# Performance work log

Measured on AMD Instinct MI355X. Metric: run time of the kernel, lower is better.

Reference implementation:

```python
import jax, jax.numpy as jnp
import numpy as np

N_GENES = 20000
HIDDEN = 64
K_HOPS = 2
N_EDGES = 640000
BATCH = 32
BN_EPS = 1e-5


def setup_inputs() -> dict:
    key = jax.random.key(0)
    ks = jax.random.split(key, 8)
    B, N, d, E = BATCH, N_GENES, HIDDEN, N_EDGES
    x = jax.random.normal(ks[0], (B, N), jnp.float32)
    edge_index = jax.random.randint(ks[1], (2, E), 0, N).astype(jnp.int64)
    gene_emb = jax.random.normal(ks[2], (N, d), jnp.float32) * 0.02
    W_sg = jax.random.normal(ks[3], (d, d), jnp.float32) / np.sqrt(d).astype(np.float32)
    b_sg = jnp.zeros((d,), jnp.float32)
    W1 = jax.random.normal(ks[4], (d, 2 * d), jnp.float32) / np.sqrt(d).astype(np.float32)
    b1 = jnp.zeros((2 * d,), jnp.float32)
    gamma1 = jnp.ones((2 * d,), jnp.float32)
    beta1 = jnp.zeros((2 * d,), jnp.float32)
    W2 = jax.random.normal(ks[5], (2 * d, 1), jnp.float32) / np.sqrt(2 * d).astype(np.float32)
    b2 = jnp.zeros((1,), jnp.float32)
    return dict(x=x, edge_index=edge_index, gene_emb=gene_emb, W_sg=W_sg, b_sg=b_sg,
                W1=W1, b1=b1, gamma1=gamma1, beta1=beta1, W2=W2, b2=b2)


def _sgconv(gene_emb, src, dst, W_sg, b_sg):
    # SGConv: h = (D^{-1/2}(A+I)D^{-1/2})^K X W  on the co-expression graph
    N = gene_emb.shape[0]
    ones = jnp.ones(src.shape, gene_emb.dtype)
    deg = jax.ops.segment_sum(ones, dst, num_segments=N) + 1.0  # +1 self loop
    dinv = jax.lax.rsqrt(deg)
    ew = dinv[src] * dinv[dst]          # [E] symmetric edge norm
    self_w = (dinv * dinv)[:, None]     # [N,1] self-loop weight
    h = gene_emb
    for _ in range(K_HOPS):
        msg = h[src] * ew[:, None]      # gather + scale  [E,d]
        h = jax.ops.segment_sum(msg, dst, num_segments=N) + h * self_w
    return h @ W_sg + b_sg              # [N,d]


def reference(x, edge_index, gene_emb, W_sg, b_sg, W1, b1, gamma1, beta1, W2, b2):
    B, N = x.shape
    src, dst = edge_index[0], edge_index[1]
    h = _sgconv(gene_emb, src, dst, W_sg, b_sg)         # [N,d]
    # per-(cell, gene) state: expression scales the gene's graph embedding
    z = (x[:, :, None] * h[None, :, :]).reshape(B * N, -1)  # [B*N, d]
    # MLP block: Linear -> BatchNorm1d (train-mode batch stats) -> ReLU -> Linear
    z = z @ W1 + b1                                     # [B*N, 2d]
    mu = jnp.mean(z, axis=0)
    var = jnp.var(z, axis=0)
    z = (z - mu) * jax.lax.rsqrt(var + BN_EPS) * gamma1 + beta1
    z = jax.nn.relu(z)
    delta = (z @ W2 + b2).reshape(B, N)                 # per-gene scalar delta
    return x + delta                                    # residual post-perturbation expression
```

## Files before the change

### kernel.cpp

```cpp
#include <hip/hip_runtime.h>
#include <hip/hip_bf16.h>

#define NG 20000
#define HD 64
#define NE 640000
#define NB 32
#define D2 128
#define BN_EPS 1e-5f

__device__ __forceinline__ unsigned pack_bf16(float x, float y) {
    unsigned ux = __float_as_uint(x), uy = __float_as_uint(y);
    unsigned lo = (ux + 0x7FFFu + ((ux >> 16) & 1u)) >> 16;
    unsigned hi = (uy + 0x7FFFu + ((uy >> 16) & 1u)) >> 16;
    return (hi << 16) | lo;
}
__device__ __forceinline__ float2 unpack_bf16(unsigned g) {
    return make_float2(__uint_as_float(g << 16), __uint_as_float(g & 0xFFFF0000u));
}

__device__ __forceinline__ void acc8(uint4 v, float& a0, float& a1, float& a2, float& a3,
                                     float& a4, float& a5, float& a6, float& a7) {
    float2 t0 = unpack_bf16(v.x), t1 = unpack_bf16(v.y);
    float2 t2 = unpack_bf16(v.z), t3 = unpack_bf16(v.w);
    a0 += t0.x; a1 += t0.y; a2 += t1.x; a3 += t1.y;
    a4 += t2.x; a5 += t2.y; a6 += t3.x; a7 += t3.y;
}

#define IB_ZC 20
#define IB_S  1
#define IB_COL 79
#define IB_WC 33

__global__ __launch_bounds__(256) void k_init(const float* __restrict__ x,
                                              const float* __restrict__ W_sg,
                                              const float* __restrict__ b_sg,
                                              const float* __restrict__ W1,
                                              int* __restrict__ cnt, float* __restrict__ S,
                                              float* __restrict__ sx, float* __restrict__ sxx,
                                              float* __restrict__ Wc, float* __restrict__ bc) {
    int blk = blockIdx.x, tid = threadIdx.x;
    if (blk < IB_ZC) {
        int i = blk * 256 + tid;
        if (i < NG / 4) ((int4*)cnt)[i] = make_int4(0, 0, 0, 0);
    } else if (blk < IB_ZC + IB_S) {
        S[tid] = 0.f;
    } else if (blk < IB_ZC + IB_S + IB_COL) {
        int n = (blk - IB_ZC - IB_S) * 256 + tid;
        if (n < NG) {
            float s = 0.f, s2 = 0.f;
            #pragma unroll
            for (int b = 0; b < NB; ++b) {
                float v = x[b * NG + n];
                s += v;
                s2 = fmaf(v, v, s2);
            }
            sx[n] = s;
            sxx[n] = s2;
        }
    } else {
        int idx = (blk - IB_ZC - IB_S - IB_COL) * 256 + tid;
        if (idx < HD * D2) {
            int k = idx >> 7, c = idx & (D2 - 1);
            float acc = 0.f;
            #pragma unroll 8
            for (int j = 0; j < HD; ++j) acc += W_sg[k * HD + j] * W1[j * D2 + c];
            Wc[idx] = acc;
        } else if (idx < HD * D2 + D2) {
            int c = idx - HD * D2;
            float acc = 0.f;
            #pragma unroll 8
            for (int j = 0; j < HD; ++j) acc += b_sg[j] * W1[j * D2 + c];
            bc[c] = acc;
        }
    }
}


__global__ void k_scatter(const int* __restrict__ src, const int* __restrict__ dst,
                          int* __restrict__ cnt, unsigned short* __restrict__ srcs) {
    int e4 = blockIdx.x * blockDim.x + threadIdx.x;
    int4 s = ((const int4*)src)[e4];
    int4 d = ((const int4*)dst)[e4];
    srcs[(d.x << 7) + atomicAdd(&cnt[d.x], 1)] = (unsigned short)s.x;
    srcs[(d.y << 7) + atomicAdd(&cnt[d.y], 1)] = (unsigned short)s.y;
    srcs[(d.z << 7) + atomicAdd(&cnt[d.z], 1)] = (unsigned short)s.z;
    srcs[(d.w << 7) + atomicAdd(&cnt[d.w], 1)] = (unsigned short)s.w;
}


__global__ __launch_bounds__(256) void k_pre(const float* __restrict__ emb,
                                             const int* __restrict__ cnt,
                                             unsigned* __restrict__ g0) {
    int i = blockIdx.x * blockDim.x + threadIdx.x;
    float dv = rsqrtf((float)cnt[i >> 3] + 1.0f);
    float4 a = ((const float4*)emb)[i * 2];
    float4 b = ((const float4*)emb)[i * 2 + 1];
    uint4 o;
    o.x = pack_bf16(a.x * dv, a.y * dv);
    o.y = pack_bf16(a.z * dv, a.w * dv);
    o.z = pack_bf16(b.x * dv, b.y * dv);
    o.w = pack_bf16(b.z * dv, b.w * dv);
    ((uint4*)g0)[i] = o;
}


__global__ __launch_bounds__(256) void k_gather1(const unsigned short* __restrict__ srcs,
                                                 const int* __restrict__ cnt,
                                                 const unsigned* __restrict__ g,
                                                 unsigned* __restrict__ outb) {
    int n = blockIdx.x * 32 + (threadIdx.x >> 3);
    int l = threadIdx.x & 7;
    const uint4* gp = (const uint4*)g + l;
    int len = cnt[n];
    const unsigned short* row = srcs + ((size_t)n << 7);
    uint4 sv = gp[(size_t)n * 8];
    float a0, a1, a2, a3, a4, a5, a6, a7;
    {
        float2 t0 = unpack_bf16(sv.x), t1 = unpack_bf16(sv.y);
        float2 t2 = unpack_bf16(sv.z), t3 = unpack_bf16(sv.w);
        a0 = t0.x; a1 = t0.y; a2 = t1.x; a3 = t1.y;
        a4 = t2.x; a5 = t2.y; a6 = t3.x; a7 = t3.y;
    }
    int j = 0;
    for (; j + 8 <= len; j += 8) {
        uint4 iw = *(const uint4*)(row + j);
        int i0 = iw.x & 0xFFFF, i1 = iw.x >> 16, i2 = iw.y & 0xFFFF, i3 = iw.y >> 16;
        int i4 = iw.z & 0xFFFF, i5 = iw.z >> 16, i6 = iw.w & 0xFFFF, i7 = iw.w >> 16;
        uint4 v0 = gp[(size_t)i0 * 8], v1 = gp[(size_t)i1 * 8];
        uint4 v2 = gp[(size_t)i2 * 8], v3 = gp[(size_t)i3 * 8];
        uint4 v4 = gp[(size_t)i4 * 8], v5 = gp[(size_t)i5 * 8];
        uint4 v6 = gp[(size_t)i6 * 8], v7 = gp[(size_t)i7 * 8];
        acc8(v0, a0, a1, a2, a3, a4, a5, a6, a7);
        acc8(v1, a0, a1, a2, a3, a4, a5, a6, a7);
        acc8(v2, a0, a1, a2, a3, a4, a5, a6, a7);
        acc8(v3, a0, a1, a2, a3, a4, a5, a6, a7);
        acc8(v4, a0, a1, a2, a3, a4, a5, a6, a7);
        acc8(v5, a0, a1, a2, a3, a4, a5, a6, a7);
        acc8(v6, a0, a1, a2, a3, a4, a5, a6, a7);
        acc8(v7, a0, a1, a2, a3, a4, a5, a6, a7);
    }
    for (; j < len; ++j) {
        uint4 v = gp[(size_t)row[j] * 8];
        acc8(v, a0, a1, a2, a3, a4, a5, a6, a7);
    }
    float dv = rsqrtf((float)len + 1.0f);
    float sc = dv * dv;
    uint4 o;
    o.x = pack_bf16(a0 * sc, a1 * sc);
    o.y = pack_bf16(a2 * sc, a3 * sc);
    o.z = pack_bf16(a4 * sc, a5 * sc);
    o.w = pack_bf16(a6 * sc, a7 * sc);
    ((uint4*)outb)[(size_t)n * 8 + l] = o;
}


__global__ __launch_bounds__(256) void k_hop2ps(const unsigned short* __restrict__ srcs,
                                                const int* __restrict__ cnt,
                                                const unsigned* __restrict__ g,
                                                const float* __restrict__ Wc,
                                                const float* __restrict__ bc,
                                                const float* __restrict__ sx,
                                                const float* __restrict__ sxx,
                                                float* __restrict__ p,
                                                float* __restrict__ S) {
    __shared__ float lWc[HD * D2];
    __shared__ float lt[HD * 32];
    int tid = threadIdx.x;
    int n0 = blockIdx.x * 32;

    for (int i = tid; i < HD * D2 / 4; i += 256)
        ((float4*)lWc)[i] = ((const float4*)Wc)[i];

    {
        int r = tid >> 3, l = tid & 7;
        int n = n0 + r;
        const uint4* gp = (const uint4*)g + l;
        int len = cnt[n];
        const unsigned short* row = srcs + ((size_t)n << 7);
        uint4 sv = gp[(size_t)n * 8];
        float a0, a1, a2, a3, a4, a5, a6, a7;
        {
            float2 t0 = unpack_bf16(sv.x), t1 = unpack_bf16(sv.y);
            float2 t2 = unpack_bf16(sv.z), t3 = unpack_bf16(sv.w);
            a0 = t0.x; a1 = t0.y; a2 = t1.x; a3 = t1.y;
            a4 = t2.x; a5 = t2.y; a6 = t3.x; a7 = t3.y;
        }
        int j = 0;
        for (; j + 8 <= len; j += 8) {
            uint4 iw = *(const uint4*)(row + j);
            int i0 = iw.x & 0xFFFF, i1 = iw.x >> 16, i2 = iw.y & 0xFFFF, i3 = iw.y >> 16;
            int i4 = iw.z & 0xFFFF, i5 = iw.z >> 16, i6 = iw.w & 0xFFFF, i7 = iw.w >> 16;
            uint4 v0 = gp[(size_t)i0 * 8], v1 = gp[(size_t)i1 * 8];
            uint4 v2 = gp[(size_t)i2 * 8], v3 = gp[(size_t)i3 * 8];
            uint4 v4 = gp[(size_t)i4 * 8], v5 = gp[(size_t)i5 * 8];
            uint4 v6 = gp[(size_t)i6 * 8], v7 = gp[(size_t)i7 * 8];
            acc8(v0, a0, a1, a2, a3, a4, a5, a6, a7);
            acc8(v1, a0, a1, a2, a3, a4, a5, a6, a7);
            acc8(v2, a0, a1, a2, a3, a4, a5, a6, a7);
            acc8(v3, a0, a1, a2, a3, a4, a5, a6, a7);
            acc8(v4, a0, a1, a2, a3, a4, a5, a6, a7);
            acc8(v5, a0, a1, a2, a3, a4, a5, a6, a7);
            acc8(v6, a0, a1, a2, a3, a4, a5, a6, a7);
            acc8(v7, a0, a1, a2, a3, a4, a5, a6, a7);
        }
        for (; j < len; ++j) {
            uint4 v = gp[(size_t)row[j] * 8];
            acc8(v, a0, a1, a2, a3, a4, a5, a6, a7);
        }
        float dv = rsqrtf((float)len + 1.0f);
        int kb = l * 8;
        lt[(kb + 0) * 32 + r] = a0 * dv;
        lt[(kb + 1) * 32 + r] = a1 * dv;
        lt[(kb + 2) * 32 + r] = a2 * dv;
        lt[(kb + 3) * 32 + r] = a3 * dv;
        lt[(kb + 4) * 32 + r] = a4 * dv;
        lt[(kb + 5) * 32 + r] = a5 * dv;
        lt[(kb + 6) * 32 + r] = a6 * dv;
        lt[(kb + 7) * 32 + r] = a7 * dv;
    }
    __syncthreads();

    int cg = tid & 31;
    int rg = tid >> 5;
    float acc[4][4];
    #pragma unroll
    for (int i = 0; i < 4; ++i)
        #pragma unroll
        for (int j = 0; j < 4; ++j) acc[i][j] = 0.f;

    #pragma unroll 4
    for (int k = 0; k < HD; ++k) {
        float4 wv = *(const float4*)&lWc[k * D2 + cg * 4];
        float4 hv = *(const float4*)&lt[k * 32 + rg * 4];
        acc[0][0] = fmaf(hv.x, wv.x, acc[0][0]);
        acc[0][1] = fmaf(hv.x, wv.y, acc[0][1]);
        acc[0][2] = fmaf(hv.x, wv.z, acc[0][2]);
        acc[0][3] = fmaf(hv.x, wv.w, acc[0][3]);
        acc[1][0] = fmaf(hv.y, wv.x, acc[1][0]);
        acc[1][1] = fmaf(hv.y, wv.y, acc[1][1]);
        acc[1][2] = fmaf(hv.y, wv.z, acc[1][2]);
        acc[1][3] = fmaf(hv.y, wv.w, acc[1][3]);
        acc[2][0] = fmaf(hv.z, wv.x, acc[2][0]);
        acc[2][1] = fmaf(hv.z, wv.y, acc[2][1]);
        acc[2][2] = fmaf(hv.z, wv.z, acc[2][2]);
        acc[2][3] = fmaf(hv.z, wv.w, acc[2][3]);
        acc[3][0] = fmaf(hv.w, wv.x, acc[3][0]);
        acc[3][1] = fmaf(hv.w, wv.y, acc[3][1]);
        acc[3][2] = fmaf(hv.w, wv.z, acc[3][2]);
        acc[3][3] = fmaf(hv.w, wv.w, acc[3][3]);
    }

    float4 bcv = ((const float4*)bc)[cg];
    float s1[4] = {0.f, 0.f, 0.f, 0.f};
    float s2[4] = {0.f, 0.f, 0.f, 0.f};
    #pragma unroll
    for (int i = 0; i < 4; ++i) {
        int rr = rg * 4 + i;
        float xs = sx[n0 + rr], xss = sxx[n0 + rr];
        float4 o;
        o.x = acc[i][0] + bcv.x;
        o.y = acc[i][1] + bcv.y;
        o.z = acc[i][2] + bcv.z;
        o.w = acc[i][3] + bcv.w;
        s1[0] = fmaf(o.x, xs, s1[0]);  s2[0] = fmaf(o.x * o.x, xss, s2[0]);
        s1[1] = fmaf(o.y, xs, s1[1]);  s2[1] = fmaf(o.y * o.y, xss, s2[1]);
        s1[2] = fmaf(o.z, xs, s1[2]);  s2[2] = fmaf(o.z * o.z, xss, s2[2]);
        s1[3] = fmaf(o.w, xs, s1[3]);  s2[3] = fmaf(o.w * o.w, xss, s2[3]);
        ((float4*)(p + (size_t)(n0 + rr) * D2))[cg] = o;
    }

    __syncthreads();
    *(float4*)&lt[rg * D2 + cg * 4]        = make_float4(s1[0], s1[1], s1[2], s1[3]);
    *(float4*)&lt[1024 + rg * D2 + cg * 4] = make_float4(s2[0], s2[1], s2[2], s2[3]);
    __syncthreads();
    if (tid < D2) {
        float a = 0.f, b = 0.f;
        #pragma unroll
        for (int g2 = 0; g2 < 8; ++g2) {
            a += lt[g2 * D2 + tid];
            b += lt[1024 + g2 * D2 + tid];
        }
        atomicAdd(&S[tid], a);
        atomicAdd(&S[D2 + tid], b);
    }
}

#define FN 64

__global__ __launch_bounds__(256) void k_final(const float* __restrict__ x,
                                               const float* __restrict__ p,
                                               const float* __restrict__ S,
                                               const float* __restrict__ gamma1,
                                               const float* __restrict__ beta1,
                                               const float* __restrict__ W2,
                                               const float* __restrict__ b2,
                                               float* __restrict__ out) {
    __shared__ float lp[FN * 129];
    __shared__ float ls[D2], lo[D2], lw[D2];
    int tid = threadIdx.x;
    int n0 = blockIdx.x * FN;
    if (tid < D2) {
        const float inv = 1.0f / (float)(NB * NG);
        float m1 = S[tid] * inv;
        float m2 = S[D2 + tid] * inv;
        float a = gamma1[tid] * rsqrtf(m2 - m1 * m1 + BN_EPS);
        ls[tid] = a;
        lo[tid] = beta1[tid] - m1 * a;
        lw[tid] = W2[tid];
    }
    for (int i = tid; i < FN * D2 / 4; i += 256) {
        int row = i >> 5, c4 = i & 31;
        int n = n0 + row;
        float4 v = (n < NG) ? ((const float4*)(p + (size_t)n * D2))[c4]
                            : make_float4(0.f, 0.f, 0.f, 0.f);
        float* dp = lp + row * 129 + c4 * 4;
        dp[0] = v.x; dp[1] = v.y; dp[2] = v.z; dp[3] = v.w;
    }
    __syncthreads();
    int nl = tid & 63;
    int n = n0 + nl;
    if (n >= NG) return;
    int bbase = (tid >> 6) * 8;
    const float* prow = lp + nl * 129;
    float b2v = b2[0];
    float xv[8], acc[8];
    #pragma unroll
    for (int bi = 0; bi < 8; ++bi) {
        xv[bi] = x[(bbase + bi) * NG + n];
        acc[bi] = 0.f;
    }
    #pragma unroll 8
    for (int c = 0; c < D2; ++c) {
        float ps = prow[c] * ls[c];
        float ocv = lo[c];
        float wv = lw[c];
        #pragma unroll
        for (int bi = 0; bi < 8; ++bi) {
            float v = fmaxf(fmaf(xv[bi], ps, ocv), 0.f);
            acc[bi] = fmaf(v, wv, acc[bi]);
        }
    }
    #pragma unroll
    for (int bi = 0; bi < 8; ++bi)
        out[(bbase + bi) * NG + n] = xv[bi] + acc[bi] + b2v;
}

extern "C" void kernel_launch(void* const* d_in, const int* in_sizes, int n_in,
                              void* d_out, int out_size, void* d_ws, size_t ws_size,
                              hipStream_t stream) {
    const float* x        = (const float*)d_in[0];
    const int*   ei       = (const int*)d_in[1];
    const float* gene_emb = (const float*)d_in[2];
    const float* W_sg     = (const float*)d_in[3];
    const float* b_sg     = (const float*)d_in[4];
    const float* W1       = (const float*)d_in[5];
    const float* gamma1   = (const float*)d_in[7];
    const float* beta1    = (const float*)d_in[8];
    const float* W2       = (const float*)d_in[9];
    const float* b2       = (const float*)d_in[10];
    float* out = (float*)d_out;

    const int* src = ei;
    const int* dst = ei + NE;

    char* base = (char*)d_ws;
    unsigned short* srcs = (unsigned short*)base;
    int*      cnt      = (int*)(base + (size_t)NG * 128 * 2);
    unsigned* g0       = (unsigned*)(cnt + NG);
    unsigned* g1       = g0 + NG * 32;
    float*    Wc       = (float*)(g1 + NG * 32);
    float*    bc       = Wc + HD * D2;
    float*    p        = bc + D2;
    float*    sx       = p + (size_t)NG * D2;
    float*    sxx      = sx + NG;
    float*    S        = sxx + NG;

    k_init<<<IB_ZC + IB_S + IB_COL + IB_WC, 256, 0, stream>>>(x, W_sg, b_sg, W1,
                                                              cnt, S, sx, sxx, Wc, bc);
    k_scatter<<<NE / 4 / 256, 256, 0, stream>>>(src, dst, cnt, srcs);
    k_pre<<<NG * HD / 8 / 256, 256, 0, stream>>>(gene_emb, cnt, g0);

    k_gather1<<<NG / 32, 256, 0, stream>>>(srcs, cnt, g0, g1);
    k_hop2ps<<<NG / 32, 256, 0, stream>>>(srcs, cnt, g1, Wc, bc, sx, sxx, p, S);

    k_final<<<(NG + FN - 1) / FN, 256, 0, stream>>>(x, p, S, gamma1, beta1, W2, b2, out);
}
```

Baseline: 174.0 us.

## Fuse all pipeline stages into one cooperative persistent kernel with grid syncs

Replaces six separate kernel launches (init, scatter, degree-normalize, hop-1 gather, hop-2 gather plus projection and statistics, final MLP) with one persistent cooperative kernel. Stages are separated by grid-wide syncs and each stage uses grid-stride loops over its work. The aim is to remove launch gaps and inter-kernel drain and fill time. In exchange, grid.sync has its own cost and occupancy is capped by the 40KB shared buffer and the launch bounds. Grid size is derived from occupancy assuming 256 CUs.

```diff
diff --git a/kernel.cpp b/kernel.cpp
--- a/kernel.cpp
+++ b/kernel.cpp
@@ -1,5 +1,8 @@
 #include <hip/hip_runtime.h>
+#include <hip/hip_cooperative_groups.h>
 #include <hip/hip_bf16.h>
+
+namespace cg = cooperative_groups;
 
 #define NG 20000
 #define HD 64
@@ -7,6 +10,9 @@
 #define NB 32
 #define D2 128
 #define BN_EPS 1e-5f
+#define FN 64
+#define NT32 625
+#define NFT 313
 
 __device__ __forceinline__ unsigned pack_bf16(float x, float y) {
     unsigned ux = __float_as_uint(x), uy = __float_as_uint(y);
@@ -17,7 +23,6 @@
 __device__ __forceinline__ float2 unpack_bf16(unsigned g) {
     return make_float2(__uint_as_float(g << 16), __uint_as_float(g & 0xFFFF0000u));
 }
-
 __device__ __forceinline__ void acc8(uint4 v, float& a0, float& a1, float& a2, float& a3,
                                      float& a4, float& a5, float& a6, float& a7) {
     float2 t0 = unpack_bf16(v.x), t1 = unpack_bf16(v.y);
@@ -26,101 +31,15 @@
     a4 += t2.x; a5 += t2.y; a6 += t3.x; a7 += t3.y;
 }
 
-#define IB_ZC 20
-#define IB_S  1
-#define IB_COL 79
-#define IB_WC 33
-
-__global__ __launch_bounds__(256) void k_init(const float* __restrict__ x,
-                                              const float* __restrict__ W_sg,
-                                              const float* __restrict__ b_sg,
-                                              const float* __restrict__ W1,
-                                              int* __restrict__ cnt, float* __restrict__ S,
-                                              float* __restrict__ sx, float* __restrict__ sxx,
-                                              float* __restrict__ Wc, float* __restrict__ bc) {
-    int blk = blockIdx.x, tid = threadIdx.x;
-    if (blk < IB_ZC) {
-        int i = blk * 256 + tid;
-        if (i < NG / 4) ((int4*)cnt)[i] = make_int4(0, 0, 0, 0);
-    } else if (blk < IB_ZC + IB_S) {
-        S[tid] = 0.f;
-    } else if (blk < IB_ZC + IB_S + IB_COL) {
-        int n = (blk - IB_ZC - IB_S) * 256 + tid;
-        if (n < NG) {
-            float s = 0.f, s2 = 0.f;
-            #pragma unroll
-            for (int b = 0; b < NB; ++b) {
-                float v = x[b * NG + n];
-                s += v;
-                s2 = fmaf(v, v, s2);
-            }
-            sx[n] = s;
-            sxx[n] = s2;
-        }
-    } else {
-        int idx = (blk - IB_ZC - IB_S - IB_COL) * 256 + tid;
-        if (idx < HD * D2) {
-            int k = idx >> 7, c = idx & (D2 - 1);
-            float acc = 0.f;
-            #pragma unroll 8
-            for (int j = 0; j < HD; ++j) acc += W_sg[k * HD + j] * W1[j * D2 + c];
-            Wc[idx] = acc;
-        } else if (idx < HD * D2 + D2) {
-            int c = idx - HD * D2;
-            float acc = 0.f;
-            #pragma unroll 8
-            for (int j = 0; j < HD; ++j) acc += b_sg[j] * W1[j * D2 + c];
-            bc[c] = acc;
-        }
-    }
-}
-
-
-__global__ void k_scatter(const int* __restrict__ src, const int* __restrict__ dst,
-                          int* __restrict__ cnt, unsigned short* __restrict__ srcs) {
-    int e4 = blockIdx.x * blockDim.x + threadIdx.x;
-    int4 s = ((const int4*)src)[e4];
-    int4 d = ((const int4*)dst)[e4];
-    srcs[(d.x << 7) + atomicAdd(&cnt[d.x], 1)] = (unsigned short)s.x;
-    srcs[(d.y << 7) + atomicAdd(&cnt[d.y], 1)] = (unsigned short)s.y;
-    srcs[(d.z << 7) + atomicAdd(&cnt[d.z], 1)] = (unsigned short)s.z;
-    srcs[(d.w << 7) + atomicAdd(&cnt[d.w], 1)] = (unsigned short)s.w;
-}
-
-
-__global__ __launch_bounds__(256) void k_pre(const float* __restrict__ emb,
-                                             const int* __restrict__ cnt,
-                                             unsigned* __restrict__ g0) {
-    int i = blockIdx.x * blockDim.x + threadIdx.x;
-    float dv = rsqrtf((float)cnt[i >> 3] + 1.0f);
-    float4 a = ((const float4*)emb)[i * 2];
-    float4 b = ((const float4*)emb)[i * 2 + 1];
-    uint4 o;
-    o.x = pack_bf16(a.x * dv, a.y * dv);
-    o.y = pack_bf16(a.z * dv, a.w * dv);
-    o.z = pack_bf16(b.x * dv, b.y * dv);
-    o.w = pack_bf16(b.z * dv, b.w * dv);
-    ((uint4*)g0)[i] = o;
-}
-
-
-__global__ __launch_bounds__(256) void k_gather1(const unsigned short* __restrict__ srcs,
-                                                 const int* __restrict__ cnt,
-                                                 const unsigned* __restrict__ g,
-                                                 unsigned* __restrict__ outb) {
-    int n = blockIdx.x * 32 + (threadIdx.x >> 3);
-    int l = threadIdx.x & 7;
-    const uint4* gp = (const uint4*)g + l;
-    int len = cnt[n];
-    const unsigned short* row = srcs + ((size_t)n << 7);
+__device__ __forceinline__ void gather_node(const unsigned short* __restrict__ row, int len,
+                                            const uint4* __restrict__ gp, int n,
+                                            float& a0, float& a1, float& a2, float& a3,
+                                            float& a4, float& a5, float& a6, float& a7) {
     uint4 sv = gp[(size_t)n * 8];
-    float a0, a1, a2, a3, a4, a5, a6, a7;
-    {
-        float2 t0 = unpack_bf16(sv.x), t1 = unpack_bf16(sv.y);
-        float2 t2 = unpack_bf16(sv.z), t3 = unpack_bf16(sv.w);
-        a0 = t0.x; a1 = t0.y; a2 = t1.x; a3 = t1.y;
-        a4 = t2.x; a5 = t2.y; a6 = t3.x; a7 = t3.y;
-    }
+    float2 t0 = unpack_bf16(sv.x), t1 = unpack_bf16(sv.y);
+    float2 t2 = unpack_bf16(sv.z), t3 = unpack_bf16(sv.w);
+    a0 = t0.x; a1 = t0.y; a2 = t1.x; a3 = t1.y;
+    a4 = t2.x; a5 = t2.y; a6 = t3.x; a7 = t3.y;
     int j = 0;
     for (; j + 8 <= len; j += 8) {
         uint4 iw = *(const uint4*)(row + j);
@@ -143,206 +62,243 @@
         uint4 v = gp[(size_t)row[j] * 8];
         acc8(v, a0, a1, a2, a3, a4, a5, a6, a7);
     }
-    float dv = rsqrtf((float)len + 1.0f);
-    float sc = dv * dv;
-    uint4 o;
-    o.x = pack_bf16(a0 * sc, a1 * sc);
-    o.y = pack_bf16(a2 * sc, a3 * sc);
-    o.z = pack_bf16(a4 * sc, a5 * sc);
-    o.w = pack_bf16(a6 * sc, a7 * sc);
-    ((uint4*)outb)[(size_t)n * 8 + l] = o;
-}
-
-
-__global__ __launch_bounds__(256) void k_hop2ps(const unsigned short* __restrict__ srcs,
-                                                const int* __restrict__ cnt,
-                                                const unsigned* __restrict__ g,
-                                                const float* __restrict__ Wc,
-                                                const float* __restrict__ bc,
-                                                const float* __restrict__ sx,
-                                                const float* __restrict__ sxx,
-                                                float* __restrict__ p,
-                                                float* __restrict__ S) {
-    __shared__ float lWc[HD * D2];
-    __shared__ float lt[HD * 32];
-    int tid = threadIdx.x;
-    int n0 = blockIdx.x * 32;
+}
+
+__global__ __launch_bounds__(256, 4) void k_all(
+        const float* __restrict__ x, const int* __restrict__ src, const int* __restrict__ dst,
+        const float* __restrict__ emb, const float* __restrict__ W_sg,
+        const float* __restrict__ b_sg, const float* __restrict__ W1,
+        const float* __restrict__ gamma1, const float* __restrict__ beta1,
+        const float* __restrict__ W2, const float* __restrict__ b2,
+        unsigned short* __restrict__ srcs, int* __restrict__ cnt,
+        unsigned* __restrict__ g0, unsigned* __restrict__ g1,
+        float* __restrict__ Wc, float* __restrict__ bc, float* __restrict__ p,
+        float* __restrict__ sx, float* __restrict__ sxx, float* __restrict__ S,
+        float* __restrict__ out) {
+    cg::grid_group grid = cg::this_grid();
+    int tid = threadIdx.x, bid = blockIdx.x, G = gridDim.x;
+    int gt = bid * 256 + tid, GT = G * 256;
+
+    __shared__ __align__(16) char smem[40960];
+    float* lWc = (float*)smem;
+    float* lt  = (float*)(smem + 32768);
+    float* lp  = (float*)smem;
+    float* ls_ = (float*)(smem + 33024);
+    float* lo_ = ls_ + D2;
+    float* lw_ = lo_ + D2;
+
+    for (int i = gt; i < NG / 4; i += GT) ((int4*)cnt)[i] = make_int4(0, 0, 0, 0);
+    for (int i = gt; i < 2 * D2; i += GT) S[i] = 0.f;
+    for (int n = gt; n < NG; n += GT) {
+        float s = 0.f, s2 = 0.f;
+        #pragma unroll
+        for (int b = 0; b < NB; ++b) {
+            float v = x[b * NG + n];
+            s += v;
+            s2 = fmaf(v, v, s2);
+        }
+        sx[n] = s;
+        sxx[n] = s2;
+    }
+    for (int idx = gt; idx < HD * D2 + D2; idx += GT) {
+        if (idx < HD * D2) {
+            int k = idx >> 7, c = idx & (D2 - 1);
+            float acc = 0.f;
+            #pragma unroll 8
+            for (int j = 0; j < HD; ++j) acc += W_sg[k * HD + j] * W1[j * D2 + c];
+            Wc[idx] = acc;
+        } else {
+            int c = idx - HD * D2;
+            float acc = 0.f;
+            #pragma unroll 8
+            for (int j = 0; j < HD; ++j) acc += b_sg[j] * W1[j * D2 + c];
+            bc[c] = acc;
+        }
+    }
+    grid.sync();
+
+    for (int e4 = gt; e4 < NE / 4; e4 += GT) {
+        int4 s = ((const int4*)src)[e4];
+        int4 d = ((const int4*)dst)[e4];
+        srcs[(d.x << 7) + atomicAdd(&cnt[d.x], 1)] = (unsigned short)s.x;
+        srcs[(d.y << 7) + atomicAdd(&cnt[d.y], 1)] = (unsigned short)s.y;
+        srcs[(d.z << 7) + atomicAdd(&cnt[d.z], 1)] = (unsigned short)s.z;
+        srcs[(d.w << 7) + atomicAdd(&cnt[d.w], 1)] = (unsigned short)s.w;
+    }
+    grid.sync();
+
+    for (int i = gt; i < NG * HD / 8; i += GT) {
+        float dv = rsqrtf((float)cnt[i >> 3] + 1.0f);
+        float4 a = ((const float4*)emb)[i * 2];
+        float4 b = ((const float4*)emb)[i * 2 + 1];
+        uint4 o;
+        o.x = pack_bf16(a.x * dv, a.y * dv);
+        o.y = pack_bf16(a.z * dv, a.w * dv);
+        o.z = pack_bf16(b.x * dv, b.y * dv);
+        o.w = pack_bf16(b.z * dv, b.w * dv);
+        ((uint4*)g0)[i] = o;
+    }
+    grid.sync();
+
+    {
+        int r = tid >> 3, l = tid & 7;
+        const uint4* gp = (const uint4*)g0 + l;
+        for (int t = bid; t < NT32; t += G) {
+            int n = t * 32 + r;
+            int len = cnt[n];
+            float a0, a1, a2, a3, a4, a5, a6, a7;
+            gather_node(srcs + ((size_t)n << 7), len, gp, n, a0, a1, a2, a3, a4, a5, a6, a7);
+            float dv = rsqrtf((float)len + 1.0f);
+            float sc = dv * dv;
+            uint4 o;
+            o.x = pack_bf16(a0 * sc, a1 * sc);
+            o.y = pack_bf16(a2 * sc, a3 * sc);
+            o.z = pack_bf16(a4 * sc, a5 * sc);
+            o.w = pack_bf16(a6 * sc, a7 * sc);
+            ((uint4*)g1)[(size_t)n * 8 + l] = o;
+        }
+    }
+    grid.sync();
 
     for (int i = tid; i < HD * D2 / 4; i += 256)
         ((float4*)lWc)[i] = ((const float4*)Wc)[i];
-
     {
         int r = tid >> 3, l = tid & 7;
-        int n = n0 + r;
-        const uint4* gp = (const uint4*)g + l;
-        int len = cnt[n];
-        const unsigned short* row = srcs + ((size_t)n << 7);
-        uint4 sv = gp[(size_t)n * 8];
-        float a0, a1, a2, a3, a4, a5, a6, a7;
-        {
-            float2 t0 = unpack_bf16(sv.x), t1 = unpack_bf16(sv.y);
-            float2 t2 = unpack_bf16(sv.z), t3 = unpack_bf16(sv.w);
-            a0 = t0.x; a1 = t0.y; a2 = t1.x; a3 = t1.y;
-            a4 = t2.x; a5 = t2.y; a6 = t3.x; a7 = t3.y;
-        }
-        int j = 0;
-        for (; j + 8 <= len; j += 8) {
-            uint4 iw = *(const uint4*)(row + j);
-            int i0 = iw.x & 0xFFFF, i1 = iw.x >> 16, i2 = iw.y & 0xFFFF, i3 = iw.y >> 16;
-            int i4 = iw.z & 0xFFFF, i5 = iw.z >> 16, i6 = iw.w & 0xFFFF, i7 = iw.w >> 16;
-            uint4 v0 = gp[(size_t)i0 * 8], v1 = gp[(size_t)i1 * 8];
-            uint4 v2 = gp[(size_t)i2 * 8], v3 = gp[(size_t)i3 * 8];
-            uint4 v4 = gp[(size_t)i4 * 8], v5 = gp[(size_t)i5 * 8];
-            uint4 v6 = gp[(size_t)i6 * 8], v7 = gp[(size_t)i7 * 8];
-            acc8(v0, a0, a1, a2, a3, a4, a5, a6, a7);
-            acc8(v1, a0, a1, a2, a3, a4, a5, a6, a7);
-            acc8(v2, a0, a1, a2, a3, a4, a5, a6, a7);
-            acc8(v3, a0, a1, a2, a3, a4, a5, a6, a7);
-            acc8(v4, a0, a1, a2, a3, a4, a5, a6, a7);
-            acc8(v5, a0, a1, a2, a3, a4, a5, a6, a7);
-            acc8(v6, a0, a1, a2, a3, a4, a5, a6, a7);
-            acc8(v7, a0, a1, a2, a3, a4, a5, a6, a7);
-        }
-        for (; j < len; ++j) {
-            uint4 v = gp[(size_t)row[j] * 8];
-            acc8(v, a0, a1, a2, a3, a4, a5, a6, a7);
-        }
-        float dv = rsqrtf((float)len + 1.0f);
-        int kb = l * 8;
-        lt[(kb + 0) * 32 + r] = a0 * dv;
-        lt[(kb + 1) * 32 + r] = a1 * dv;
-        lt[(kb + 2) * 32 + r] = a2 * dv;
-        lt[(kb + 3) * 32 + r] = a3 * dv;
-        lt[(kb + 4) * 32 + r] = a4 * dv;
-        lt[(kb + 5) * 32 + r] = a5 * dv;
-        lt[(kb + 6) * 32 + r] = a6 * dv;
-        lt[(kb + 7) * 32 + r] = a7 * dv;
-    }
-    __syncthreads();
-
-    int cg = tid & 31;
-    int rg = tid >> 5;
-    float acc[4][4];
-    #pragma unroll
-    for (int i = 0; i < 4; ++i)
-        #pragma unroll
-        for (int j = 0; j < 4; ++j) acc[i][j] = 0.f;
-
-    #pragma unroll 4
-    for (int k = 0; k < HD; ++k) {
-        float4 wv = *(const float4*)&lWc[k * D2 + cg * 4];
-        float4 hv = *(const float4*)&lt[k * 32 + rg * 4];
-        acc[0][0] = fmaf(hv.x, wv.x, acc[0][0]);
-        acc[0][1] = fmaf(hv.x, wv.y, acc[0][1]);
-        acc[0][2] = fmaf(hv.x, wv.z, acc[0][2]);
-        acc[0][3] = fmaf(hv.x, wv.w, acc[0][3]);
-        acc[1][0] = fmaf(hv.y, wv.x, acc[1][0]);
-        acc[1][1] = fmaf(hv.y, wv.y, acc[1][1]);
-        acc[1][2] = fmaf(hv.y, wv.z, acc[1][2]);
-        acc[1][3] = fmaf(hv.y, wv.w, acc[1][3]);
-        acc[2][0] = fmaf(hv.z, wv.x, acc[2][0]);
-        acc[2][1] = fmaf(hv.z, wv.y, acc[2][1]);
-        acc[2][2] = fmaf(hv.z, wv.z, acc[2][2]);
-        acc[2][3] = fmaf(hv.z, wv.w, acc[2][3]);
-        acc[3][0] = fmaf(hv.w, wv.x, acc[3][0]);
-        acc[3][1] = fmaf(hv.w, wv.y, acc[3][1]);
-        acc[3][2] = fmaf(hv.w, wv.z, acc[3][2]);
-        acc[3][3] = fmaf(hv.w, wv.w, acc[3][3]);
-    }
-
-    float4 bcv = ((const float4*)bc)[cg];
-    float s1[4] = {0.f, 0.f, 0.f, 0.f};
-    float s2[4] = {0.f, 0.f, 0.f, 0.f};
-    #pragma unroll
-    for (int i = 0; i < 4; ++i) {
-        int rr = rg * 4 + i;
-        float xs = sx[n0 + rr], xss = sxx[n0 + rr];
-        float4 o;
-        o.x = acc[i][0] + bcv.x;
-        o.y = acc[i][1] + bcv.y;
-        o.z = acc[i][2] + bcv.z;
-        o.w = acc[i][3] + bcv.w;
-        s1[0] = fmaf(o.x, xs, s1[0]);  s2[0] = fmaf(o.x * o.x, xss, s2[0]);
-        s1[1] = fmaf(o.y, xs, s1[1]);  s2[1] = fmaf(o.y * o.y, xss, s2[1]);
-        s1[2] = fmaf(o.z, xs, s1[2]);  s2[2] = fmaf(o.z * o.z, xss, s2[2]);
-        s1[3] = fmaf(o.w, xs, s1[3]);  s2[3] = fmaf(o.w * o.w, xss, s2[3]);
-        ((float4*)(p + (size_t)(n0 + rr) * D2))[cg] = o;
-    }
-
-    __syncthreads();
-    *(float4*)&lt[rg * D2 + cg * 4]        = make_float4(s1[0], s1[1], s1[2], s1[3]);
-    *(float4*)&lt[1024 + rg * D2 + cg * 4] = make_float4(s2[0], s2[1], s2[2], s2[3]);
-    __syncthreads();
-    if (tid < D2) {
-        float a = 0.f, b = 0.f;
-        #pragma unroll
-        for (int g2 = 0; g2 < 8; ++g2) {
-            a += lt[g2 * D2 + tid];
-            b += lt[1024 + g2 * D2 + tid];
-        }
-        atomicAdd(&S[tid], a);
-        atomicAdd(&S[D2 + tid], b);
-    }
-}
-
-#define FN 64
-
-__global__ __launch_bounds__(256) void k_final(const float* __restrict__ x,
-                                               const float* __restrict__ p,
-                                               const float* __restrict__ S,
-                                               const float* __restrict__ gamma1,
-                                               const float* __restrict__ beta1,
-                                               const float* __restrict__ W2,
-                                               const float* __restrict__ b2,
-                                               float* __restrict__ out) {
-    __shared__ float lp[FN * 129];
-    __shared__ float ls[D2], lo[D2], lw[D2];
-    int tid = threadIdx.x;
-    int n0 = blockIdx.x * FN;
+        int cgc = tid & 31, rg = tid >> 5;
+        const uint4* gp = (const uint4*)g1 + l;
+        float s1[4] = {0.f, 0.f, 0.f, 0.f};
+        float s2[4] = {0.f, 0.f, 0.f, 0.f};
+        for (int t = bid; t < NT32; t += G) {
+            int n0 = t * 32;
+            __syncthreads();
+            {
+                int n = n0 + r;
+                int len = cnt[n];
+                float a0, a1, a2, a3, a4, a5, a6, a7;
+                gather_node(srcs + ((size_t)n << 7), len, gp, n, a0, a1, a2, a3, a4, a5, a6, a7);
+                float dv = rsqrtf((float)len + 1.0f);
+                int kb = l * 8;
+                lt[(kb + 0) * 32 + r] = a0 * dv;
+                lt[(kb + 1) * 32 + r] = a1 * dv;
+                lt[(kb + 2) * 32 + r] = a2 * dv;
+                lt[(kb + 3) * 32 + r] = a3 * dv;
+                lt[(kb + 4) * 32 + r] = a4 * dv;
+                lt[(kb + 5) * 32 + r] = a5 * dv;
+                lt[(kb + 6) * 32 + r] = a6 * dv;
+                lt[(kb + 7) * 32 + r] = a7 * dv;
+            }
+            __syncthreads();
+            float acc[4][4];
+            #pragma unroll
+            for (int i = 0; i < 4; ++i)
+                #pragma unroll
+                for (int j = 0; j < 4; ++j) acc[i][j] = 0.f;
+            #pragma unroll 4
+            for (int k = 0; k < HD; ++k) {
+                float4 wv = *(const float4*)&lWc[k * D2 + cgc * 4];
+                float4 hv = *(const float4*)&lt[k * 32 + rg * 4];
+                acc[0][0] = fmaf(hv.x, wv.x, acc[0][0]);
+                acc[0][1] = fmaf(hv.x, wv.y, acc[0][1]);
+                acc[0][2] = fmaf(hv.x, wv.z, acc[0][2]);
+                acc[0][3] = fmaf(hv.x, wv.w, acc[0][3]);
+                acc[1][0] = fmaf(hv.y, wv.x, acc[1][0]);
+                acc[1][1] = fmaf(hv.y, wv.y, acc[1][1]);
+                acc[1][2] = fmaf(hv.y, wv.z, acc[1][2]);
+                acc[1][3] = fmaf(hv.y, wv.w, acc[1][3]);
+                acc[2][0] = fmaf(hv.z, wv.x, acc[2][0]);
+                acc[2][1] = fmaf(hv.z, wv.y, acc[2][1]);
+                acc[2][2] = fmaf(hv.z, wv.z, acc[2][2]);
+                acc[2][3] = fmaf(hv.z, wv.w, acc[2][3]);
+                acc[3][0] = fmaf(hv.w, wv.x, acc[3][0]);
+                acc[3][1] = fmaf(hv.w, wv.y, acc[3][1]);
+                acc[3][2] = fmaf(hv.w, wv.z, acc[3][2]);
+                acc[3][3] = fmaf(hv.w, wv.w, acc[3][3]);
+            }
+            float4 bcv = ((const float4*)bc)[cgc];
+            #pragma unroll
+            for (int i = 0; i < 4; ++i) {
+                int rr = rg * 4 + i;
+                float xs = sx[n0 + rr], xss = sxx[n0 + rr];
+                float4 o;
+                o.x = acc[i][0] + bcv.x;
+                o.y = acc[i][1] + bcv.y;
+                o.z = acc[i][2] + bcv.z;
+                o.w = acc[i][3] + bcv.w;
+                s1[0] = fmaf(o.x, xs, s1[0]);  s2[0] = fmaf(o.x * o.x, xss, s2[0]);
+                s1[1] = fmaf(o.y, xs, s1[1]);  s2[1] = fmaf(o.y * o.y, xss, s2[1]);
+                s1[2] = fmaf(o.z, xs, s1[2]);  s2[2] = fmaf(o.z * o.z, xss, s2[2]);
+                s1[3] = fmaf(o.w, xs, s1[3]);  s2[3] = fmaf(o.w * o.w, xss, s2[3]);
+                ((float4*)(p + (size_t)(n0 + rr) * D2))[cgc] = o;
+            }
+        }
+        __syncthreads();
+        *(float4*)&lt[rg * D2 + cgc * 4]        = make_float4(s1[0], s1[1], s1[2], s1[3]);
+        *(float4*)&lt[1024 + rg * D2 + cgc * 4] = make_float4(s2[0], s2[1], s2[2], s2[3]);
+        __syncthreads();
+        if (tid < D2) {
+            float a = 0.f, b = 0.f;
+            #pragma unroll
+            for (int g2 = 0; g2 < 8; ++g2) {
+                a += lt[g2 * D2 + tid];
+                b += lt[1024 + g2 * D2 + tid];
+            }
+            atomicAdd(&S[tid], a);
+            atomicAdd(&S[D2 + tid], b);
+        }
+    }
+    grid.sync();
+
     if (tid < D2) {
         const float inv = 1.0f / (float)(NB * NG);
         float m1 = S[tid] * inv;
         float m2 = S[D2 + tid] * inv;
         float a = gamma1[tid] * rsqrtf(m2 - m1 * m1 + BN_EPS);
-        ls[tid] = a;
-        lo[tid] = beta1[tid] - m1 * a;
-        lw[tid] = W2[tid];
-    }
-    for (int i = tid; i < FN * D2 / 4; i += 256) {
-        int row = i >> 5, c4 = i & 31;
-        int n = n0 + row;
-        float4 v = (n < NG) ? ((const float4*)(p + (size_t)n * D2))[c4]
-                            : make_float4(0.f, 0.f, 0.f, 0.f);
-        float* dp = lp + row * 129 + c4 * 4;
-        dp[0] = v.x; dp[1] = v.y; dp[2] = v.z; dp[3] = v.w;
-    }
-    __syncthreads();
-    int nl = tid & 63;
-    int n = n0 + nl;
-    if (n >= NG) return;
-    int bbase = (tid >> 6) * 8;
-    const float* prow = lp + nl * 129;
-    float b2v = b2[0];
-    float xv[8], acc[8];
-    #pragma unroll
-    for (int bi = 0; bi < 8; ++bi) {
-        xv[bi] = x[(bbase + bi) * NG + n];
-        acc[bi] = 0.f;
-    }
-    #pragma unroll 8
-    for (int c = 0; c < D2; ++c) {
-        float ps = prow[c] * ls[c];
-        float ocv = lo[c];
-        float wv = lw[c];
-        #pragma unroll
-        for (int bi = 0; bi < 8; ++bi) {
-            float v = fmaxf(fmaf(xv[bi], ps, ocv), 0.f);
-            acc[bi] = fmaf(v, wv, acc[bi]);
-        }
-    }
-    #pragma unroll
-    for (int bi = 0; bi < 8; ++bi)
-        out[(bbase + bi) * NG + n] = xv[bi] + acc[bi] + b2v;
+        ls_[tid] = a;
+        lo_[tid] = beta1[tid] - m1 * a;
+        lw_[tid] = W2[tid];
+    }
+    {
+        int nl = tid & 63;
+        int bbase = (tid >> 6) * 8;
+        float b2v = b2[0];
+        for (int t = bid; t < NFT; t += G) {
+            int n0 = t * FN;
+            __syncthreads();
+            for (int i = tid; i < FN * D2 / 4; i += 256) {
+                int row = i >> 5, c4 = i & 31;
+                int n = n0 + row;
+                float4 v = (n < NG) ? ((const float4*)(p + (size_t)n * D2))[c4]
+                                    : make_float4(0.f, 0.f, 0.f, 0.f);
+                float* dp = lp + row * 129 + c4 * 4;
+                dp[0] = v.x; dp[1] = v.y; dp[2] = v.z; dp[3] = v.w;
+            }
+            __syncthreads();
+            int n = n0 + nl;
+            if (n < NG) {
+                const float* prow = lp + nl * 129;
+                float xv[8], acc[8];
+                #pragma unroll
+                for (int bi = 0; bi < 8; ++bi) {
+                    xv[bi] = x[(bbase + bi) * NG + n];
+                    acc[bi] = 0.f;
+                }
+                #pragma unroll 8
+                for (int c = 0; c < D2; ++c) {
+                    float ps = prow[c] * ls_[c];
+                    float ocv = lo_[c];
+                    float wv = lw_[c];
+                    #pragma unroll
+                    for (int bi = 0; bi < 8; ++bi) {
+                        float v = fmaxf(fmaf(xv[bi], ps, ocv), 0.f);
+                        acc[bi] = fmaf(v, wv, acc[bi]);
+                    }
+                }
+                #pragma unroll
+                for (int bi = 0; bi < 8; ++bi)
+                    out[(bbase + bi) * NG + n] = xv[bi] + acc[bi] + b2v;
+            }
+        }
+    }
 }
 
 extern "C" void kernel_launch(void* const* d_in, const int* in_sizes, int n_in,
@@ -375,13 +331,18 @@
     float*    sxx      = sx + NG;
     float*    S        = sxx + NG;
 
-    k_init<<<IB_ZC + IB_S + IB_COL + IB_WC, 256, 0, stream>>>(x, W_sg, b_sg, W1,
-                                                              cnt, S, sx, sxx, Wc, bc);
-    k_scatter<<<NE / 4 / 256, 256, 0, stream>>>(src, dst, cnt, srcs);
-    k_pre<<<NG * HD / 8 / 256, 256, 0, stream>>>(gene_emb, cnt, g0);
-
-    k_gather1<<<NG / 32, 256, 0, stream>>>(srcs, cnt, g0, g1);
-    k_hop2ps<<<NG / 32, 256, 0, stream>>>(srcs, cnt, g1, Wc, bc, sx, sxx, p, S);
-
-    k_final<<<(NG + FN - 1) / FN, 256, 0, stream>>>(x, p, S, gamma1, beta1, W2, b2, out);
-}
+    int bpc = 0;
+    hipOccupancyMaxActiveBlocksPerMultiprocessor(&bpc, k_all, 256, 0);
+    if (bpc < 1) bpc = 1;
+    int grid = bpc * 256;
+    if (grid > 1024) grid = 1024;
+
+    void* args[] = {
+        (void*)&x, (void*)&src, (void*)&dst, (void*)&gene_emb, (void*)&W_sg,
+        (void*)&b_sg, (void*)&W1, (void*)&gamma1, (void*)&beta1, (void*)&W2,
+        (void*)&b2, (void*)&srcs, (void*)&cnt, (void*)&g0, (void*)&g1,
+        (void*)&Wc, (void*)&bc, (void*)&p, (void*)&sx, (void*)&sxx,
+        (void*)&S, (void*)&out
+    };
+    hipLaunchCooperativeKernel((const void*)k_all, dim3(grid), dim3(256), args, 0, stream);
+}
```

Result: slower. 468.6 us (+169.4%).
